# Kernel optimization log

Measured on AMD Instinct MI355X. Metric: run time of the kernel, lower is better.

The kernel has to match this reference:

```python
import jax, jax.numpy as jnp
import numpy as np

B, T, D = 2, 2048, 1024
H = 16
HD = D // H  # 64


def setup_inputs() -> dict:
    key = jax.random.key(0)
    k1, k2, k3, k4, k5 = jax.random.split(key, 5)
    s = 0.02
    return {
        "x": jax.random.normal(k1, (B, T, D), dtype=jnp.float32),
        "Wqkv": jax.random.normal(k2, (D, 3 * D), dtype=jnp.float32) * s,
        "bqkv": jax.random.normal(k3, (3 * D,), dtype=jnp.float32) * s,
        "Wout": jax.random.normal(k4, (D, D), dtype=jnp.float32) * s,
        "bout": jax.random.normal(k5, (D,), dtype=jnp.float32) * s,
    }


def reference(x, Wqkv, bqkv, Wout, bout):
    b, t, c = x.shape
    qkv = (x @ Wqkv + bqkv).reshape(b, t, 3, H, HD)
    q = jnp.transpose(qkv[:, :, 0], (0, 2, 1, 3))  # [B,H,T,HD]
    k = jnp.transpose(qkv[:, :, 1], (0, 2, 1, 3))
    v = jnp.transpose(qkv[:, :, 2], (0, 2, 1, 3))
    att = jnp.einsum("bhqd,bhkd->bhqk", q, k) * (HD ** -0.5)
    mask = jnp.tril(jnp.ones((t, t), dtype=bool))  # causal, no past kv
    att = jnp.where(mask, att, -jnp.inf)
    att = jax.nn.softmax(att, axis=-1)
    y = jnp.einsum("bhqk,bhkd->bhqd", att, v)
    y = jnp.transpose(y, (0, 2, 1, 3)).reshape(b, t, c)
    return y @ Wout + bout
```

## Files before the change

kernel.cpp:

```cpp
#include <hip/hip_runtime.h>
#include <hip/hip_bf16.h>
#include <math.h>

#define B_  2
#define T_  2048
#define D_  1024
#define H_  16
#define HD_ 64

typedef __attribute__((ext_vector_type(8))) short short8;
typedef __attribute__((ext_vector_type(4))) float f32x4;

#if __has_builtin(__builtin_amdgcn_exp2f)
#define EXP2F __builtin_amdgcn_exp2f
#else
#define EXP2F exp2f
#endif

__device__ __forceinline__ ushort f2bf(float x) {
    unsigned u = __builtin_bit_cast(unsigned, x);
    return (ushort)((u + 0x7FFFu + ((u >> 16) & 1u)) >> 16);
}

__device__ __forceinline__ unsigned pack_bf2_fast(float a, float b) {
    unsigned ua = __builtin_bit_cast(unsigned, a) + 0x8000u;
    unsigned ub = __builtin_bit_cast(unsigned, b) + 0x8000u;
    return (ua >> 16) | (ub & 0xFFFF0000u);
}

__device__ __forceinline__ void load_lds_16B(const ushort* g, ushort* l) {
    __builtin_amdgcn_global_load_lds(
        (const __attribute__((address_space(1))) unsigned*)g,
        (__attribute__((address_space(3))) unsigned*)l, 16, 0, 0);
}

__global__ __launch_bounds__(256)
void prep_kernel(const float* __restrict__ x, ushort* __restrict__ xb,
                 const float* __restrict__ Wqkv, ushort* __restrict__ Wqkvt,
                 const float* __restrict__ Wout, ushort* __restrict__ Woutt)
{
    __shared__ ushort Ts[64][65];
    const int bid = blockIdx.x;

    if (bid < 512) {
        const int n4 = (B_ * T_ * D_) / 4;
        for (int i = bid * 256 + threadIdx.x; i < n4; i += 512 * 256) {
            float4 v = ((const float4*)x)[i];
            ushort4 o = { f2bf(v.x), f2bf(v.y), f2bf(v.z), f2bf(v.w) };
            ((ushort4*)xb)[i] = o;
        }
        return;
    }

    const float* W; ushort* Wt; int K, M, m0, k0;
    if (bid < 1280) {
        const int t = bid - 512;
        W = Wqkv; Wt = Wqkvt; K = D_; M = 3 * D_;
        m0 = (t % 48) * 64; k0 = (t / 48) * 64;
    } else {
        const int t = bid - 1280;
        W = Wout; Wt = Woutt; K = D_; M = D_;
        m0 = (t % 16) * 64; k0 = (t / 16) * 64;
    }

    const int tr = threadIdx.x >> 4;
    const int tc = threadIdx.x & 15;
    #pragma unroll
    for (int it = 0; it < 4; it++) {
        int k = tr + it * 16;
        float4 v = *(const float4*)&W[(size_t)(k0 + k) * M + m0 + tc * 4];
        Ts[tc * 4 + 0][k] = f2bf(v.x);
        Ts[tc * 4 + 1][k] = f2bf(v.y);
        Ts[tc * 4 + 2][k] = f2bf(v.z);
        Ts[tc * 4 + 3][k] = f2bf(v.w);
    }
    __syncthreads();
    #pragma unroll
    for (int it = 0; it < 2; it++) {
        const int mr  = (threadIdx.x >> 3) + it * 32;
        const int seg = (threadIdx.x & 7) * 8;
        short8 v;
        #pragma unroll
        for (int r = 0; r < 8; r++) v[r] = (short)Ts[mr][seg + r];
        *(short8*)&Wt[(size_t)(m0 + mr) * K + k0 + seg] = v;
    }
}

__global__ __launch_bounds__(256, 4)
void gemm_qkv(const ushort* __restrict__ A, const ushort* __restrict__ Bt,
              const float* __restrict__ bias,
              ushort* __restrict__ Qg, ushort* __restrict__ Kg,
              ushort* __restrict__ Vtg)
{
    const int K = D_;
    __shared__ __align__(16) ushort lds[16384];
    ushort* Asl = lds;
    ushort* Bsl = lds + 8192;

    const int tid = threadIdx.x;
    const int w  = tid >> 6, L = tid & 63;
    const int lt = L & 15, lq = L >> 4;
    const int wr = w >> 1, wc = w & 1;
    const int m0 = blockIdx.x * 128, n0 = blockIdx.y * 128;
    const int rsub = L >> 3;
    const int pgr  = L & 7;

    f32x4 acc[4][4] = {};

    for (int k0 = 0; k0 < K; k0 += 64) {
        __syncthreads();
        #pragma unroll
        for (int j = 0; j < 4; j++) {
            const int row  = (w * 4 + j) * 8 + rsub;
            const int gran = pgr ^ rsub;
            load_lds_16B(A  + (size_t)(n0 + row) * K + k0 + gran * 8,
                         &Asl[row * 64 + pgr * 8]);
            load_lds_16B(Bt + (size_t)(m0 + row) * K + k0 + gran * 8,
                         &Bsl[row * 64 + pgr * 8]);
        }
        __syncthreads();

        #pragma unroll
        for (int ks = 0; ks < 2; ks++) {
            short8 af[4], bf[4];
            #pragma unroll
            for (int i = 0; i < 4; i++) {
                const int ra = wr * 64 + i * 16 + lt;
                af[i] = *(const short8*)&Asl[ra * 64 + (((ks * 4 + lq) ^ (ra & 7)) * 8)];
                const int rb = wc * 64 + i * 16 + lt;
                bf[i] = *(const short8*)&Bsl[rb * 64 + (((ks * 4 + lq) ^ (rb & 7)) * 8)];
            }
            #pragma unroll
            for (int i = 0; i < 4; i++)
                #pragma unroll
                for (int j = 0; j < 4; j++)
                    acc[i][j] = __builtin_amdgcn_mfma_f32_16x16x32_bf16(af[i], bf[j], acc[i][j], 0, 0, 0);
        }
    }

    __syncthreads();
    const int s  = m0 >> 10;
    const int h0 = (m0 & 1023) >> 6;
    const float qs = (s == 0) ? 0.18033688011112042f : 1.0f;

    if (s < 2) {
        #pragma unroll
        for (int j = 0; j < 4; j++) {
            const int m  = wc * 64 + j * 16 + lt;
            const float bv = bias[m0 + m];
            #pragma unroll
            for (int i = 0; i < 4; i++) {
                const int n = wr * 64 + i * 16 + lq * 4;
                #pragma unroll
                for (int r = 0; r < 4; r++)
                    lds[(n + r) * 128 + m] = f2bf((acc[i][j][r] + bv) * qs);
            }
        }
        __syncthreads();
        ushort* dst = (s == 0 ? Qg : Kg);
        #pragma unroll
        for (int it = 0; it < 8; it++) {
            const int g   = tid + it * 256;
            const int row = g >> 4, c = g & 15;
            const int n = n0 + row;
            const int b = n >> 11, t = n & 2047;
            const int h = h0 + (c >> 3), d = (c & 7) * 8;
            short8 v = *(const short8*)&lds[row * 128 + c * 8];
            *(short8*)&dst[((size_t)(b * H_ + h) * T_ + t) * HD_ + d] = v;
        }
    } else {
        #pragma unroll
        for (int j = 0; j < 4; j++) {
            const int m  = wc * 64 + j * 16 + lt;
            const float bv = bias[m0 + m];
            #pragma unroll
            for (int i = 0; i < 4; i++) {
                const int n = wr * 64 + i * 16 + lq * 4;
                uint2 pk = { pack_bf2_fast(acc[i][j][0] + bv, acc[i][j][1] + bv),
                             pack_bf2_fast(acc[i][j][2] + bv, acc[i][j][3] + bv) };
                *(uint2*)&lds[m * 128 + n] = pk;
            }
        }
        __syncthreads();
        const int b = n0 >> 11, t0 = n0 & 2047;
        #pragma unroll
        for (int it = 0; it < 8; it++) {
            const int g   = tid + it * 256;
            const int row = g >> 4, c = g & 15;
            const int h = h0 + (row >> 6), d = row & 63;
            short8 v = *(const short8*)&lds[row * 128 + c * 8];
            *(short8*)&Vtg[((size_t)(b * H_ + h) * HD_ + d) * T_ + t0 + c * 8] = v;
        }
    }
}

__global__ __launch_bounds__(256, 4)
void gemm_out(const ushort* __restrict__ A, const ushort* __restrict__ Bt,
              const float* __restrict__ bias, float* __restrict__ C)
{
    const int K = D_, M = D_;
    __shared__ __align__(16) ushort lds[8192 + 4096];
    ushort* Asl = lds;
    ushort* Bsl = lds + 8192;

    const int tid = threadIdx.x;
    const int w  = tid >> 6, L = tid & 63;
    const int lt = L & 15, lq = L >> 4;
    const int wr = w >> 1, wc = w & 1;
    const int m0 = blockIdx.x * 64, n0 = blockIdx.y * 128;
    const int rsub = L >> 3;
    const int pgr  = L & 7;

    f32x4 acc[2][4] = {};

    for (int k0 = 0; k0 < K; k0 += 64) {
        __syncthreads();
        #pragma unroll
        for (int j = 0; j < 4; j++) {
            const int row  = (w * 4 + j) * 8 + rsub;
            const int gran = pgr ^ rsub;
            load_lds_16B(A + (size_t)(n0 + row) * K + k0 + gran * 8,
                         &Asl[row * 64 + pgr * 8]);
        }
        #pragma unroll
        for (int j = 0; j < 2; j++) {
            const int row  = (w * 2 + j) * 8 + rsub;
            const int gran = pgr ^ rsub;
            load_lds_16B(Bt + (size_t)(m0 + row) * K + k0 + gran * 8,
                         &Bsl[row * 64 + pgr * 8]);
        }
        __syncthreads();

        #pragma unroll
        for (int ks = 0; ks < 2; ks++) {
            short8 wf[2], yf[4];
            #pragma unroll
            for (int j = 0; j < 2; j++) {
                const int rb = wc * 32 + j * 16 + lt;
                wf[j] = *(const short8*)&Bsl[rb * 64 + (((ks * 4 + lq) ^ (rb & 7)) * 8)];
            }
            #pragma unroll
            for (int i = 0; i < 4; i++) {
                const int ra = wr * 64 + i * 16 + lt;
                yf[i] = *(const short8*)&Asl[ra * 64 + (((ks * 4 + lq) ^ (ra & 7)) * 8)];
            }
            #pragma unroll
            for (int j = 0; j < 2; j++)
                #pragma unroll
                for (int i = 0; i < 4; i++)
                    acc[j][i] = __builtin_amdgcn_mfma_f32_16x16x32_bf16(wf[j], yf[i], acc[j][i], 0, 0, 0);
        }
    }

    #pragma unroll
    for (int j = 0; j < 2; j++) {
        const int mbase = m0 + wc * 32 + j * 16 + lq * 4;
        const float4 bv = *(const float4*)&bias[mbase];
        #pragma unroll
        for (int i = 0; i < 4; i++) {
            const int n = n0 + wr * 64 + i * 16 + lt;
            float4 o = { acc[j][i][0] + bv.x, acc[j][i][1] + bv.y,
                         acc[j][i][2] + bv.z, acc[j][i][3] + bv.w };
            *(float4*)&C[(size_t)n * M + mbase] = o;
        }
    }
}

__global__ __launch_bounds__(256, 4)
void attn_mfma(const ushort* __restrict__ Qg, const ushort* __restrict__ Kg,
               const ushort* __restrict__ Vtg, ushort* __restrict__ yb)
{
    const int h = blockIdx.y, b = blockIdx.z;
    const int flip = ((blockIdx.y >> 3) ^ blockIdx.z) & 1;
    const int qb = flip ? blockIdx.x : (31 - blockIdx.x);
    const int tid = threadIdx.x;
    const int w  = tid >> 6, L = tid & 63;
    const int lt = L & 15, lq = L >> 4;
    const int kswz = lt & 7;

    __shared__ __align__(16) ushort Ks [128 * 64];
    __shared__ __align__(16) ushort Vts[64 * 128];
    __shared__ __align__(16) ushort Ps [4][16 * 40];

    const size_t bh = (size_t)(b * H_ + h);
    const ushort* Qbase  = Qg  + bh * T_ * HD_;
    const ushort* Kbase  = Kg  + bh * T_ * HD_;
    const ushort* Vtbase = Vtg + bh * HD_ * T_;

    const int q_glob = qb * 64 + w * 16 + lt;
    const short8 qf0 = *(const short8*)(Qbase + (size_t)q_glob * HD_ + lq * 8);
    const short8 qf1 = *(const short8*)(Qbase + (size_t)q_glob * HD_ + 32 + lq * 8);

    f32x4 acc_o[4] = {};
    float lsum = 0.f;

    const int krow = tid >> 3, kpg = tid & 7;
    const int vrow = tid >> 4, vpg = tid & 15;
    const int nk = (qb + 2) >> 1;

    for (int kb = 0; kb < nk; kb++) {
        __syncthreads();
        #pragma unroll
        for (int rr = 0; rr < 4; rr++) {
            const int row = krow + 32 * rr;
            load_lds_16B(Kbase + (size_t)(kb * 128 + row) * HD_ + (kpg ^ (row & 7)) * 8,
                         &Ks[row * 64 + kpg * 8]);
        }
        #pragma unroll
        for (int rr = 0; rr < 4; rr++) {
            const int d = vrow + 16 * rr;
            load_lds_16B(Vtbase + (size_t)d * T_ + kb * 128 + (vpg ^ (d & 7)) * 8,
                         &Vts[d * 128 + vpg * 8]);
        }
        __syncthreads();

        if (kb < nk - 1) {
            #pragma unroll
            for (int ks = 0; ks < 4; ks++) {
                const int row0 = (2 * ks) * 16 + lt;
                const int row1 = row0 + 16;
                short8 a00 = *(const short8*)&Ks[row0 * 64 + ((lq ^ kswz) * 8)];
                short8 a01 = *(const short8*)&Ks[row0 * 64 + (((4 + lq) ^ kswz) * 8)];
                short8 a10 = *(const short8*)&Ks[row1 * 64 + ((lq ^ kswz) * 8)];
                short8 a11 = *(const short8*)&Ks[row1 * 64 + (((4 + lq) ^ kswz) * 8)];
                f32x4 c0 = {}, c1 = {};
                c0 = __builtin_amdgcn_mfma_f32_16x16x32_bf16(a00, qf0, c0, 0, 0, 0);
                c0 = __builtin_amdgcn_mfma_f32_16x16x32_bf16(a01, qf1, c0, 0, 0, 0);
                c1 = __builtin_amdgcn_mfma_f32_16x16x32_bf16(a10, qf0, c1, 0, 0, 0);
                c1 = __builtin_amdgcn_mfma_f32_16x16x32_bf16(a11, qf1, c1, 0, 0, 0);

                float p0 = EXP2F(c0[0]), p1 = EXP2F(c0[1]);
                float p2 = EXP2F(c0[2]), p3 = EXP2F(c0[3]);
                float p4 = EXP2F(c1[0]), p5 = EXP2F(c1[1]);
                float p6 = EXP2F(c1[2]), p7 = EXP2F(c1[3]);
                lsum += ((p0 + p1) + (p2 + p3)) + ((p4 + p5) + (p6 + p7));
                uint2 pk0 = { pack_bf2_fast(p0, p1), pack_bf2_fast(p2, p3) };
                uint2 pk1 = { pack_bf2_fast(p4, p5), pack_bf2_fast(p6, p7) };
                *(uint2*)&Ps[w][lt * 40 + lq * 4]      = pk0;
                *(uint2*)&Ps[w][lt * 40 + 16 + lq * 4] = pk1;

                short8 pf = *(const short8*)&Ps[w][lt * 40 + lq * 8];

                #pragma unroll
                for (int dt = 0; dt < 4; dt++) {
                    const int vr = dt * 16 + lt;
                    short8 vf = *(const short8*)&Vts[vr * 128 + (((ks * 4 + lq) ^ kswz) * 8)];
                    acc_o[dt] = __builtin_amdgcn_mfma_f32_16x16x32_bf16(pf, vf, acc_o[dt], 0, 0, 0);
                }
            }
        } else {
            const int ksN = (qb & 1) ? 4 : 2;
            const int mk0 = (qb & 1) ? 2 : 0;
            for (int ks = 0; ks < ksN; ks++) {
                const int row0 = (2 * ks) * 16 + lt;
                const int row1 = row0 + 16;
                short8 a00 = *(const short8*)&Ks[row0 * 64 + ((lq ^ kswz) * 8)];
                short8 a01 = *(const short8*)&Ks[row0 * 64 + (((4 + lq) ^ kswz) * 8)];
                short8 a10 = *(const short8*)&Ks[row1 * 64 + ((lq ^ kswz) * 8)];
                short8 a11 = *(const short8*)&Ks[row1 * 64 + (((4 + lq) ^ kswz) * 8)];
                f32x4 c0 = {}, c1 = {};
                c0 = __builtin_amdgcn_mfma_f32_16x16x32_bf16(a00, qf0, c0, 0, 0, 0);
                c0 = __builtin_amdgcn_mfma_f32_16x16x32_bf16(a01, qf1, c0, 0, 0, 0);
                c1 = __builtin_amdgcn_mfma_f32_16x16x32_bf16(a10, qf0, c1, 0, 0, 0);
                c1 = __builtin_amdgcn_mfma_f32_16x16x32_bf16(a11, qf1, c1, 0, 0, 0);

                float p[8];
                #pragma unroll
                for (int r = 0; r < 4; r++) { p[r] = EXP2F(c0[r]); p[4 + r] = EXP2F(c1[r]); }
                if (ks >= mk0) {
                    const int key0 = kb * 128 + (2 * ks) * 16 + lq * 4;
                    #pragma unroll
                    for (int r = 0; r < 4; r++) {
                        if (key0 + r > q_glob)      p[r] = 0.f;
                        if (key0 + 16 + r > q_glob) p[4 + r] = 0.f;
                    }
                }
                lsum += ((p[0] + p[1]) + (p[2] + p[3])) + ((p[4] + p[5]) + (p[6] + p[7]));
                uint2 pk0 = { pack_bf2_fast(p[0], p[1]), pack_bf2_fast(p[2], p[3]) };
                uint2 pk1 = { pack_bf2_fast(p[4], p[5]), pack_bf2_fast(p[6], p[7]) };
                *(uint2*)&Ps[w][lt * 40 + lq * 4]      = pk0;
                *(uint2*)&Ps[w][lt * 40 + 16 + lq * 4] = pk1;

                short8 pf = *(const short8*)&Ps[w][lt * 40 + lq * 8];

                #pragma unroll
                for (int dt = 0; dt < 4; dt++) {
                    const int vr = dt * 16 + lt;
                    short8 vf = *(const short8*)&Vts[vr * 128 + (((ks * 4 + lq) ^ kswz) * 8)];
                    acc_o[dt] = __builtin_amdgcn_mfma_f32_16x16x32_bf16(pf, vf, acc_o[dt], 0, 0, 0);
                }
            }
        }
    }

    lsum += __shfl_xor(lsum, 16, 64);
    lsum += __shfl_xor(lsum, 32, 64);
    const float inv = 1.0f / lsum;

    float linv[4];
    #pragma unroll
    for (int r = 0; r < 4; r++) linv[r] = __shfl(inv, lq * 4 + r, 64);

    ushort* ybase = yb + (size_t)(b * T_ + qb * 64 + w * 16) * D_ + h * HD_;
    #pragma unroll
    for (int r = 0; r < 4; r++)
        #pragma unroll
        for (int dt = 0; dt < 4; dt++)
            ybase[(size_t)(lq * 4 + r) * D_ + dt * 16 + lt] = f2bf(acc_o[dt][r] * linv[r]);
}

extern "C" void kernel_launch(void* const* d_in, const int* in_sizes, int n_in,
                              void* d_out, int out_size, void* d_ws, size_t ws_size,
                              hipStream_t stream)
{
    const float* x    = (const float*)d_in[0];
    const float* Wqkv = (const float*)d_in[1];
    const float* bqkv = (const float*)d_in[2];
    const float* Wout = (const float*)d_in[3];
    const float* bout = (const float*)d_in[4];
    float* out = (float*)d_out;

    char* ws = (char*)d_ws;
    const size_t NT = (size_t)B_ * T_;
    ushort* xb     = (ushort*)ws;
    ushort* Wqkvt  = (ushort*)(ws + NT * D_ * 2);
    ushort* Woutt  = (ushort*)(ws + NT * D_ * 2 + (size_t)3 * D_ * D_ * 2);
    char*   p      = ws + NT * D_ * 2 + (size_t)4 * D_ * D_ * 2;
    const size_t qkv_elems = (size_t)B_ * H_ * T_ * HD_;
    ushort* Qg  = (ushort*)p;
    ushort* Kg  = (ushort*)(p + qkv_elems * 2);
    ushort* Vtg = (ushort*)(p + qkv_elems * 4);
    ushort* yb  = (ushort*)(p + qkv_elems * 6);

    prep_kernel<<<1536, 256, 0, stream>>>(x, xb, Wqkv, Wqkvt, Wout, Woutt);

    gemm_qkv<<<dim3(3 * D_ / 128, NT / 128), 256, 0, stream>>>(
        xb, Wqkvt, bqkv, Qg, Kg, Vtg);

    attn_mfma<<<dim3(32, H_, B_), 256, 0, stream>>>(Qg, Kg, Vtg, yb);

    gemm_out<<<dim3(D_ / 64, NT / 128), 256, 0, stream>>>(
        yb, Woutt, bout, out);
}
```

Before: 168.8 us.

## Process two 64-row query tiles per attention block to reuse K/V tiles

```diff
diff --git a/kernel.cpp b/kernel.cpp
--- a/kernel.cpp
+++ b/kernel.cpp
@@ -266,13 +266,13 @@
     }
 }
 
-__global__ __launch_bounds__(256, 4)
+__global__ __launch_bounds__(256, 2)
 void attn_mfma(const ushort* __restrict__ Qg, const ushort* __restrict__ Kg,
                const ushort* __restrict__ Vtg, ushort* __restrict__ yb)
 {
     const int h = blockIdx.y, b = blockIdx.z;
     const int flip = ((blockIdx.y >> 3) ^ blockIdx.z) & 1;
-    const int qb = flip ? blockIdx.x : (31 - blockIdx.x);
+    const int qb = flip ? blockIdx.x : (15 - blockIdx.x);
     const int tid = threadIdx.x;
     const int w  = tid >> 6, L = tid & 63;
     const int lt = L & 15, lq = L >> 4;
@@ -280,25 +280,27 @@
 
     __shared__ __align__(16) ushort Ks [128 * 64];
     __shared__ __align__(16) ushort Vts[64 * 128];
-    __shared__ __align__(16) ushort Ps [4][16 * 40];
+    __shared__ __align__(16) ushort Ps [4][2][16 * 40];
 
     const size_t bh = (size_t)(b * H_ + h);
     const ushort* Qbase  = Qg  + bh * T_ * HD_;
     const ushort* Kbase  = Kg  + bh * T_ * HD_;
     const ushort* Vtbase = Vtg + bh * HD_ * T_;
 
-    const int q_glob = qb * 64 + w * 16 + lt;
-    const short8 qf0 = *(const short8*)(Qbase + (size_t)q_glob * HD_ + lq * 8);
-    const short8 qf1 = *(const short8*)(Qbase + (size_t)q_glob * HD_ + 32 + lq * 8);
-
-    f32x4 acc_o[4] = {};
-    float lsum = 0.f;
+    const int q0 = qb * 128 + w * 16 + lt;
+    const int q1 = q0 + 64;
+    const short8 qf00 = *(const short8*)(Qbase + (size_t)q0 * HD_ + lq * 8);
+    const short8 qf01 = *(const short8*)(Qbase + (size_t)q0 * HD_ + 32 + lq * 8);
+    const short8 qf10 = *(const short8*)(Qbase + (size_t)q1 * HD_ + lq * 8);
+    const short8 qf11 = *(const short8*)(Qbase + (size_t)q1 * HD_ + 32 + lq * 8);
+
+    f32x4 acc0[4] = {}, acc1[4] = {};
+    float lsum0 = 0.f, lsum1 = 0.f;
 
     const int krow = tid >> 3, kpg = tid & 7;
     const int vrow = tid >> 4, vpg = tid & 15;
-    const int nk = (qb + 2) >> 1;
-
-    for (int kb = 0; kb < nk; kb++) {
+
+    for (int kb = 0; kb <= qb; kb++) {
         __syncthreads();
         #pragma unroll
         for (int rr = 0; rr < 4; rr++) {
@@ -314,99 +316,94 @@
         }
         __syncthreads();
 
-        if (kb < nk - 1) {
-            #pragma unroll
-            for (int ks = 0; ks < 4; ks++) {
-                const int row0 = (2 * ks) * 16 + lt;
-                const int row1 = row0 + 16;
-                short8 a00 = *(const short8*)&Ks[row0 * 64 + ((lq ^ kswz) * 8)];
-                short8 a01 = *(const short8*)&Ks[row0 * 64 + (((4 + lq) ^ kswz) * 8)];
-                short8 a10 = *(const short8*)&Ks[row1 * 64 + ((lq ^ kswz) * 8)];
-                short8 a11 = *(const short8*)&Ks[row1 * 64 + (((4 + lq) ^ kswz) * 8)];
-                f32x4 c0 = {}, c1 = {};
-                c0 = __builtin_amdgcn_mfma_f32_16x16x32_bf16(a00, qf0, c0, 0, 0, 0);
-                c0 = __builtin_amdgcn_mfma_f32_16x16x32_bf16(a01, qf1, c0, 0, 0, 0);
-                c1 = __builtin_amdgcn_mfma_f32_16x16x32_bf16(a10, qf0, c1, 0, 0, 0);
-                c1 = __builtin_amdgcn_mfma_f32_16x16x32_bf16(a11, qf1, c1, 0, 0, 0);
-
-                float p0 = EXP2F(c0[0]), p1 = EXP2F(c0[1]);
-                float p2 = EXP2F(c0[2]), p3 = EXP2F(c0[3]);
-                float p4 = EXP2F(c1[0]), p5 = EXP2F(c1[1]);
-                float p6 = EXP2F(c1[2]), p7 = EXP2F(c1[3]);
-                lsum += ((p0 + p1) + (p2 + p3)) + ((p4 + p5) + (p6 + p7));
-                uint2 pk0 = { pack_bf2_fast(p0, p1), pack_bf2_fast(p2, p3) };
-                uint2 pk1 = { pack_bf2_fast(p4, p5), pack_bf2_fast(p6, p7) };
-                *(uint2*)&Ps[w][lt * 40 + lq * 4]      = pk0;
-                *(uint2*)&Ps[w][lt * 40 + 16 + lq * 4] = pk1;
-
-                short8 pf = *(const short8*)&Ps[w][lt * 40 + lq * 8];
-
+        const bool lastkb = (kb == qb);
+        #pragma unroll
+        for (int ks = 0; ks < 4; ks++) {
+            const int row0 = (2 * ks) * 16 + lt;
+            const int row1 = row0 + 16;
+            short8 a00 = *(const short8*)&Ks[row0 * 64 + ((lq ^ kswz) * 8)];
+            short8 a01 = *(const short8*)&Ks[row0 * 64 + (((4 + lq) ^ kswz) * 8)];
+            short8 a10 = *(const short8*)&Ks[row1 * 64 + ((lq ^ kswz) * 8)];
+            short8 a11 = *(const short8*)&Ks[row1 * 64 + (((4 + lq) ^ kswz) * 8)];
+            f32x4 c00 = {}, c01 = {}, c10 = {}, c11 = {};
+            __builtin_amdgcn_s_setprio(1);
+            c00 = __builtin_amdgcn_mfma_f32_16x16x32_bf16(a00, qf00, c00, 0, 0, 0);
+            c00 = __builtin_amdgcn_mfma_f32_16x16x32_bf16(a01, qf01, c00, 0, 0, 0);
+            c01 = __builtin_amdgcn_mfma_f32_16x16x32_bf16(a10, qf00, c01, 0, 0, 0);
+            c01 = __builtin_amdgcn_mfma_f32_16x16x32_bf16(a11, qf01, c01, 0, 0, 0);
+            c10 = __builtin_amdgcn_mfma_f32_16x16x32_bf16(a00, qf10, c10, 0, 0, 0);
+            c10 = __builtin_amdgcn_mfma_f32_16x16x32_bf16(a01, qf11, c10, 0, 0, 0);
+            c11 = __builtin_amdgcn_mfma_f32_16x16x32_bf16(a10, qf10, c11, 0, 0, 0);
+            c11 = __builtin_amdgcn_mfma_f32_16x16x32_bf16(a11, qf11, c11, 0, 0, 0);
+            __builtin_amdgcn_s_setprio(0);
+
+            float p0[8], p1[8];
+            #pragma unroll
+            for (int r = 0; r < 4; r++) {
+                p0[r]     = EXP2F(c00[r]);
+                p0[4 + r] = EXP2F(c01[r]);
+                p1[r]     = EXP2F(c10[r]);
+                p1[4 + r] = EXP2F(c11[r]);
+            }
+            if (lastkb) {
+                const int key0 = kb * 128 + (2 * ks) * 16 + lq * 4;
                 #pragma unroll
-                for (int dt = 0; dt < 4; dt++) {
-                    const int vr = dt * 16 + lt;
-                    short8 vf = *(const short8*)&Vts[vr * 128 + (((ks * 4 + lq) ^ kswz) * 8)];
-                    acc_o[dt] = __builtin_amdgcn_mfma_f32_16x16x32_bf16(pf, vf, acc_o[dt], 0, 0, 0);
+                for (int r = 0; r < 4; r++) {
+                    if (key0 + r > q0)      p0[r]     = 0.f;
+                    if (key0 + 16 + r > q0) p0[4 + r] = 0.f;
+                    if (key0 + r > q1)      p1[r]     = 0.f;
+                    if (key0 + 16 + r > q1) p1[4 + r] = 0.f;
                 }
             }
-        } else {
-            const int ksN = (qb & 1) ? 4 : 2;
-            const int mk0 = (qb & 1) ? 2 : 0;
-            for (int ks = 0; ks < ksN; ks++) {
-                const int row0 = (2 * ks) * 16 + lt;
-                const int row1 = row0 + 16;
-                short8 a00 = *(const short8*)&Ks[row0 * 64 + ((lq ^ kswz) * 8)];
-                short8 a01 = *(const short8*)&Ks[row0 * 64 + (((4 + lq) ^ kswz) * 8)];
-                short8 a10 = *(const short8*)&Ks[row1 * 64 + ((lq ^ kswz) * 8)];
-                short8 a11 = *(const short8*)&Ks[row1 * 64 + (((4 + lq) ^ kswz) * 8)];
-                f32x4 c0 = {}, c1 = {};
-                c0 = __builtin_amdgcn_mfma_f32_16x16x32_bf16(a00, qf0, c0, 0, 0, 0);
-                c0 = __builtin_amdgcn_mfma_f32_16x16x32_bf16(a01, qf1, c0, 0, 0, 0);
-                c1 = __builtin_amdgcn_mfma_f32_16x16x32_bf16(a10, qf0, c1, 0, 0, 0);
-                c1 = __builtin_amdgcn_mfma_f32_16x16x32_bf16(a11, qf1, c1, 0, 0, 0);
-
-                float p[8];
-                #pragma unroll
-                for (int r = 0; r < 4; r++) { p[r] = EXP2F(c0[r]); p[4 + r] = EXP2F(c1[r]); }
-                if (ks >= mk0) {
-                    const int key0 = kb * 128 + (2 * ks) * 16 + lq * 4;
-                    #pragma unroll
-                    for (int r = 0; r < 4; r++) {
-                        if (key0 + r > q_glob)      p[r] = 0.f;
-                        if (key0 + 16 + r > q_glob) p[4 + r] = 0.f;
-                    }
-                }
-                lsum += ((p[0] + p[1]) + (p[2] + p[3])) + ((p[4] + p[5]) + (p[6] + p[7]));
-                uint2 pk0 = { pack_bf2_fast(p[0], p[1]), pack_bf2_fast(p[2], p[3]) };
-                uint2 pk1 = { pack_bf2_fast(p[4], p[5]), pack_bf2_fast(p[6], p[7]) };
-                *(uint2*)&Ps[w][lt * 40 + lq * 4]      = pk0;
-                *(uint2*)&Ps[w][lt * 40 + 16 + lq * 4] = pk1;
-
-                short8 pf = *(const short8*)&Ps[w][lt * 40 + lq * 8];
-
-                #pragma unroll
-                for (int dt = 0; dt < 4; dt++) {
-                    const int vr = dt * 16 + lt;
-                    short8 vf = *(const short8*)&Vts[vr * 128 + (((ks * 4 + lq) ^ kswz) * 8)];
-                    acc_o[dt] = __builtin_amdgcn_mfma_f32_16x16x32_bf16(pf, vf, acc_o[dt], 0, 0, 0);
-                }
-            }
-        }
-    }
-
-    lsum += __shfl_xor(lsum, 16, 64);
-    lsum += __shfl_xor(lsum, 32, 64);
-    const float inv = 1.0f / lsum;
-
-    float linv[4];
+            lsum0 += ((p0[0] + p0[1]) + (p0[2] + p0[3])) + ((p0[4] + p0[5]) + (p0[6] + p0[7]));
+            lsum1 += ((p1[0] + p1[1]) + (p1[2] + p1[3])) + ((p1[4] + p1[5]) + (p1[6] + p1[7]));
+            uint2 pk00 = { pack_bf2_fast(p0[0], p0[1]), pack_bf2_fast(p0[2], p0[3]) };
+            uint2 pk01 = { pack_bf2_fast(p0[4], p0[5]), pack_bf2_fast(p0[6], p0[7]) };
+            uint2 pk10 = { pack_bf2_fast(p1[0], p1[1]), pack_bf2_fast(p1[2], p1[3]) };
+            uint2 pk11 = { pack_bf2_fast(p1[4], p1[5]), pack_bf2_fast(p1[6], p1[7]) };
+            *(uint2*)&Ps[w][0][lt * 40 + lq * 4]      = pk00;
+            *(uint2*)&Ps[w][0][lt * 40 + 16 + lq * 4] = pk01;
+            *(uint2*)&Ps[w][1][lt * 40 + lq * 4]      = pk10;
+            *(uint2*)&Ps[w][1][lt * 40 + 16 + lq * 4] = pk11;
+
+            short8 pf0 = *(const short8*)&Ps[w][0][lt * 40 + lq * 8];
+            short8 pf1 = *(const short8*)&Ps[w][1][lt * 40 + lq * 8];
+
+            __builtin_amdgcn_s_setprio(1);
+            #pragma unroll
+            for (int dt = 0; dt < 4; dt++) {
+                const int vr = dt * 16 + lt;
+                short8 vf = *(const short8*)&Vts[vr * 128 + (((ks * 4 + lq) ^ kswz) * 8)];
+                acc0[dt] = __builtin_amdgcn_mfma_f32_16x16x32_bf16(pf0, vf, acc0[dt], 0, 0, 0);
+                acc1[dt] = __builtin_amdgcn_mfma_f32_16x16x32_bf16(pf1, vf, acc1[dt], 0, 0, 0);
+            }
+            __builtin_amdgcn_s_setprio(0);
+        }
+    }
+
+    lsum0 += __shfl_xor(lsum0, 16, 64);
+    lsum0 += __shfl_xor(lsum0, 32, 64);
+    lsum1 += __shfl_xor(lsum1, 16, 64);
+    lsum1 += __shfl_xor(lsum1, 32, 64);
+    const float inv0 = 1.0f / lsum0;
+    const float inv1 = 1.0f / lsum1;
+
+    float linv0[4], linv1[4];
     #pragma unroll
-    for (int r = 0; r < 4; r++) linv[r] = __shfl(inv, lq * 4 + r, 64);
-
-    ushort* ybase = yb + (size_t)(b * T_ + qb * 64 + w * 16) * D_ + h * HD_;
+    for (int r = 0; r < 4; r++) {
+        linv0[r] = __shfl(inv0, lq * 4 + r, 64);
+        linv1[r] = __shfl(inv1, lq * 4 + r, 64);
+    }
+
+    ushort* y0 = yb + (size_t)(b * T_ + qb * 128 + w * 16) * D_ + h * HD_;
+    ushort* y1 = y0 + (size_t)64 * D_;
     #pragma unroll
     for (int r = 0; r < 4; r++)
         #pragma unroll
-        for (int dt = 0; dt < 4; dt++)
-            ybase[(size_t)(lq * 4 + r) * D_ + dt * 16 + lt] = f2bf(acc_o[dt][r] * linv[r]);
+        for (int dt = 0; dt < 4; dt++) {
+            y0[(size_t)(lq * 4 + r) * D_ + dt * 16 + lt] = f2bf(acc0[dt][r] * linv0[r]);
+            y1[(size_t)(lq * 4 + r) * D_ + dt * 16 + lt] = f2bf(acc1[dt][r] * linv1[r]);
+        }
 }
 
 extern "C" void kernel_launch(void* const* d_in, const int* in_sizes, int n_in,
@@ -437,7 +434,7 @@
     gemm_qkv<<<dim3(3 * D_ / 128, NT / 128), 256, 0, stream>>>(
         xb, Wqkvt, bqkv, Qg, Kg, Vtg);
 
-    attn_mfma<<<dim3(32, H_, B_), 256, 0, stream>>>(Qg, Kg, Vtg, yb);
+    attn_mfma<<<dim3(16, H_, B_), 256, 0, stream>>>(Qg, Kg, Vtg, yb);
 
     gemm_out<<<dim3(D_ / 64, NT / 128), 256, 0, stream>>>(
         yb, Woutt, bout, out);
```

After: 176.0 us. 4.3% more time.

## Remap key rows so P stays in registers, dropping the LDS round-trip

Applied to the files above, without the earlier changes.

```diff
diff --git a/kernel.cpp b/kernel.cpp
--- a/kernel.cpp
+++ b/kernel.cpp
@@ -10,6 +10,7 @@
 
 typedef __attribute__((ext_vector_type(8))) short short8;
 typedef __attribute__((ext_vector_type(4))) float f32x4;
+typedef __attribute__((ext_vector_type(4))) unsigned uint32x4;
 
 #if __has_builtin(__builtin_amdgcn_exp2f)
 #define EXP2F __builtin_amdgcn_exp2f
@@ -280,7 +281,6 @@
 
     __shared__ __align__(16) ushort Ks [128 * 64];
     __shared__ __align__(16) ushort Vts[64 * 128];
-    __shared__ __align__(16) ushort Ps [4][16 * 40];
 
     const size_t bh = (size_t)(b * H_ + h);
     const ushort* Qbase  = Qg  + bh * T_ * HD_;
@@ -303,7 +303,8 @@
         #pragma unroll
         for (int rr = 0; rr < 4; rr++) {
             const int row = krow + 32 * rr;
-            load_lds_16B(Kbase + (size_t)(kb * 128 + row) * HD_ + (kpg ^ (row & 7)) * 8,
+            const int swzK = (((row >> 3) & 1) * 4) | (row & 3);
+            load_lds_16B(Kbase + (size_t)(kb * 128 + row) * HD_ + (kpg ^ swzK) * 8,
                          &Ks[row * 64 + kpg * 8]);
         }
         #pragma unroll
@@ -314,82 +315,49 @@
         }
         __syncthreads();
 
-        if (kb < nk - 1) {
-            #pragma unroll
-            for (int ks = 0; ks < 4; ks++) {
-                const int row0 = (2 * ks) * 16 + lt;
-                const int row1 = row0 + 16;
-                short8 a00 = *(const short8*)&Ks[row0 * 64 + ((lq ^ kswz) * 8)];
-                short8 a01 = *(const short8*)&Ks[row0 * 64 + (((4 + lq) ^ kswz) * 8)];
-                short8 a10 = *(const short8*)&Ks[row1 * 64 + ((lq ^ kswz) * 8)];
-                short8 a11 = *(const short8*)&Ks[row1 * 64 + (((4 + lq) ^ kswz) * 8)];
-                f32x4 c0 = {}, c1 = {};
-                c0 = __builtin_amdgcn_mfma_f32_16x16x32_bf16(a00, qf0, c0, 0, 0, 0);
-                c0 = __builtin_amdgcn_mfma_f32_16x16x32_bf16(a01, qf1, c0, 0, 0, 0);
-                c1 = __builtin_amdgcn_mfma_f32_16x16x32_bf16(a10, qf0, c1, 0, 0, 0);
-                c1 = __builtin_amdgcn_mfma_f32_16x16x32_bf16(a11, qf1, c1, 0, 0, 0);
-
-                float p0 = EXP2F(c0[0]), p1 = EXP2F(c0[1]);
-                float p2 = EXP2F(c0[2]), p3 = EXP2F(c0[3]);
-                float p4 = EXP2F(c1[0]), p5 = EXP2F(c1[1]);
-                float p6 = EXP2F(c1[2]), p7 = EXP2F(c1[3]);
-                lsum += ((p0 + p1) + (p2 + p3)) + ((p4 + p5) + (p6 + p7));
-                uint2 pk0 = { pack_bf2_fast(p0, p1), pack_bf2_fast(p2, p3) };
-                uint2 pk1 = { pack_bf2_fast(p4, p5), pack_bf2_fast(p6, p7) };
-                *(uint2*)&Ps[w][lt * 40 + lq * 4]      = pk0;
-                *(uint2*)&Ps[w][lt * 40 + 16 + lq * 4] = pk1;
-
-                short8 pf = *(const short8*)&Ps[w][lt * 40 + lq * 8];
-
+        const bool lastkb = (kb == nk - 1);
+        const int ksN = (!lastkb) ? 4 : ((qb & 1) ? 4 : 2);
+        const int mk0 = (qb & 1) ? 2 : 0;
+        for (int ks = 0; ks < ksN; ks++) {
+            const int row0 = ks * 32 + ((lt >> 2) * 8) + (lt & 3);
+            const int row1 = row0 + 4;
+            short8 a00 = *(const short8*)&Ks[row0 * 64 + ((lq ^ kswz) * 8)];
+            short8 a01 = *(const short8*)&Ks[row0 * 64 + (((4 + lq) ^ kswz) * 8)];
+            short8 a10 = *(const short8*)&Ks[row1 * 64 + ((lq ^ kswz) * 8)];
+            short8 a11 = *(const short8*)&Ks[row1 * 64 + (((4 + lq) ^ kswz) * 8)];
+            f32x4 c0 = {}, c1 = {};
+            __builtin_amdgcn_s_setprio(1);
+            c0 = __builtin_amdgcn_mfma_f32_16x16x32_bf16(a00, qf0, c0, 0, 0, 0);
+            c0 = __builtin_amdgcn_mfma_f32_16x16x32_bf16(a01, qf1, c0, 0, 0, 0);
+            c1 = __builtin_amdgcn_mfma_f32_16x16x32_bf16(a10, qf0, c1, 0, 0, 0);
+            c1 = __builtin_amdgcn_mfma_f32_16x16x32_bf16(a11, qf1, c1, 0, 0, 0);
+            __builtin_amdgcn_s_setprio(0);
+
+            float p[8];
+            #pragma unroll
+            for (int r = 0; r < 4; r++) { p[r] = EXP2F(c0[r]); p[4 + r] = EXP2F(c1[r]); }
+            if (lastkb && ks >= mk0) {
+                const int key0 = kb * 128 + ks * 32 + lq * 8;
                 #pragma unroll
-                for (int dt = 0; dt < 4; dt++) {
-                    const int vr = dt * 16 + lt;
-                    short8 vf = *(const short8*)&Vts[vr * 128 + (((ks * 4 + lq) ^ kswz) * 8)];
-                    acc_o[dt] = __builtin_amdgcn_mfma_f32_16x16x32_bf16(pf, vf, acc_o[dt], 0, 0, 0);
+                for (int r = 0; r < 4; r++) {
+                    if (key0 + r > q_glob)     p[r]     = 0.f;
+                    if (key0 + 4 + r > q_glob) p[4 + r] = 0.f;
                 }
             }
-        } else {
-            const int ksN = (qb & 1) ? 4 : 2;
-            const int mk0 = (qb & 1) ? 2 : 0;
-            for (int ks = 0; ks < ksN; ks++) {
-                const int row0 = (2 * ks) * 16 + lt;
-                const int row1 = row0 + 16;
-                short8 a00 = *(const short8*)&Ks[row0 * 64 + ((lq ^ kswz) * 8)];
-                short8 a01 = *(const short8*)&Ks[row0 * 64 + (((4 + lq) ^ kswz) * 8)];
-                short8 a10 = *(const short8*)&Ks[row1 * 64 + ((lq ^ kswz) * 8)];
-                short8 a11 = *(const short8*)&Ks[row1 * 64 + (((4 + lq) ^ kswz) * 8)];
-                f32x4 c0 = {}, c1 = {};
-                c0 = __builtin_amdgcn_mfma_f32_16x16x32_bf16(a00, qf0, c0, 0, 0, 0);
-                c0 = __builtin_amdgcn_mfma_f32_16x16x32_bf16(a01, qf1, c0, 0, 0, 0);
-                c1 = __builtin_amdgcn_mfma_f32_16x16x32_bf16(a10, qf0, c1, 0, 0, 0);
-                c1 = __builtin_amdgcn_mfma_f32_16x16x32_bf16(a11, qf1, c1, 0, 0, 0);
-
-                float p[8];
-                #pragma unroll
-                for (int r = 0; r < 4; r++) { p[r] = EXP2F(c0[r]); p[4 + r] = EXP2F(c1[r]); }
-                if (ks >= mk0) {
-                    const int key0 = kb * 128 + (2 * ks) * 16 + lq * 4;
-                    #pragma unroll
-                    for (int r = 0; r < 4; r++) {
-                        if (key0 + r > q_glob)      p[r] = 0.f;
-                        if (key0 + 16 + r > q_glob) p[4 + r] = 0.f;
-                    }
-                }
-                lsum += ((p[0] + p[1]) + (p[2] + p[3])) + ((p[4] + p[5]) + (p[6] + p[7]));
-                uint2 pk0 = { pack_bf2_fast(p[0], p[1]), pack_bf2_fast(p[2], p[3]) };
-                uint2 pk1 = { pack_bf2_fast(p[4], p[5]), pack_bf2_fast(p[6], p[7]) };
-                *(uint2*)&Ps[w][lt * 40 + lq * 4]      = pk0;
-                *(uint2*)&Ps[w][lt * 40 + 16 + lq * 4] = pk1;
-
-                short8 pf = *(const short8*)&Ps[w][lt * 40 + lq * 8];
-
-                #pragma unroll
-                for (int dt = 0; dt < 4; dt++) {
-                    const int vr = dt * 16 + lt;
-                    short8 vf = *(const short8*)&Vts[vr * 128 + (((ks * 4 + lq) ^ kswz) * 8)];
-                    acc_o[dt] = __builtin_amdgcn_mfma_f32_16x16x32_bf16(pf, vf, acc_o[dt], 0, 0, 0);
-                }
-            }
+            lsum += ((p[0] + p[1]) + (p[2] + p[3])) + ((p[4] + p[5]) + (p[6] + p[7]));
+
+            uint32x4 pw = { pack_bf2_fast(p[0], p[1]), pack_bf2_fast(p[2], p[3]),
+                            pack_bf2_fast(p[4], p[5]), pack_bf2_fast(p[6], p[7]) };
+            short8 pf = __builtin_bit_cast(short8, pw);
+
+            __builtin_amdgcn_s_setprio(1);
+            #pragma unroll
+            for (int dt = 0; dt < 4; dt++) {
+                const int vr = dt * 16 + lt;
+                short8 vf = *(const short8*)&Vts[vr * 128 + (((ks * 4 + lq) ^ kswz) * 8)];
+                acc_o[dt] = __builtin_amdgcn_mfma_f32_16x16x32_bf16(pf, vf, acc_o[dt], 0, 0, 0);
+            }
+            __builtin_amdgcn_s_setprio(0);
         }
     }
 
```

New measurement: 168.9 us. Within noise of the previous version (+0.1%).
